# Performance work log

Hardware: AMD Instinct MI355X
Metric: run time of the kernel (lower is better)

Reference implementation:

```python
import jax, jax.numpy as jnp
import numpy as np

N, C = 65536, 512
DK = C // 2
B = 1024  # crystals; L = N // B atoms per crystal
BN_EPS = 1e-5
L1_EPS = 1e-9


def setup_inputs() -> dict:
    key = jax.random.key(0)
    ks = jax.random.split(key, 4)
    s = 1.0 / np.sqrt(C)
    return {
        "atom_fea": jax.random.normal(ks[0], (N, C), jnp.float32),
        # q_conv and k_conv share weight/bias in the original module -> single Wqk
        "Wqk": jax.random.normal(ks[1], (DK, C), jnp.float32) * s,
        "bqk": jnp.zeros((DK,), jnp.float32),
        "Wv": jax.random.normal(ks[2], (C, C), jnp.float32) * s,
        "bv": jnp.zeros((C,), jnp.float32),
        "Wt": jax.random.normal(ks[3], (C, C), jnp.float32) * s,
        "bt": jnp.zeros((C,), jnp.float32),
        "gamma": jnp.ones((C,), jnp.float32),
        "beta": jnp.zeros((C,), jnp.float32),
        "num_crystals": B,
    }


def reference(atom_fea, Wqk, bqk, Wv, bv, Wt, bt, gamma, beta, num_crystals):
    n, c = atom_fea.shape
    dk = Wqk.shape[0]
    b = num_crystals
    l = n // b  # atoms per crystal (equal-size segments)

    # 1x1 convs == linear projections; q and k are tied -> one projection
    qk = atom_fea @ Wqk.T + bqk          # [N, dk]
    v = atom_fea @ Wv.T + bv             # [N, C]

    qkb = qk.reshape(b, l, dk)
    vb = v.reshape(b, l, c)

    # per-crystal energy: [b, i(query), j(key)]
    energy = jnp.einsum("bid,bjd->bij", qkb, qkb) / jnp.sqrt(jnp.float32(dk))
    # softmax over dim=-2 (query axis), then L1-normalize over keys
    a = jax.nn.softmax(energy, axis=-2)
    att = a / (L1_EPS + a.sum(axis=-1, keepdims=True))

    x_r = jnp.einsum("bij,bjc->bic", att, vb).reshape(n, c)
    x_trans = atom_fea - x_r

    t = x_trans @ Wt.T + bt              # trans_conv (1x1)
    # BatchNorm1d in training mode: batch stats over the atom axis
    mean = t.mean(axis=0)
    var = t.var(axis=0)
    bn = (t - mean) * jax.lax.rsqrt(var + BN_EPS) * gamma + beta
    return atom_fea + jax.nn.relu(bn)
```

## Files before the change

### kernel.cpp

```cpp
#include <hip/hip_runtime.h>
#include <stdint.h>

#define NAT 65536
#define CH 512
#define NQKV 768

typedef __bf16 bf16x8 __attribute__((ext_vector_type(8)));
typedef float f32x4 __attribute__((ext_vector_type(4)));

union B8 { uint4 u; __bf16 h[8]; };

__device__ __forceinline__ void gload16(const void* g, void* l) {
  __builtin_amdgcn_global_load_lds((const __attribute__((address_space(1))) void*)g,
                                   (__attribute__((address_space(3))) void*)l, 16, 0, 0);
}

__global__ void k_prep(const float* __restrict__ atom, const float* __restrict__ wqk,
                       const float* __restrict__ bqk, const float* __restrict__ wv,
                       const float* __restrict__ bv, const float* __restrict__ wt,
                       __bf16* __restrict__ atom16, __bf16* __restrict__ wqkv16,
                       float* __restrict__ bqkv, __bf16* __restrict__ wt16,
                       float* __restrict__ stats)
{
  int tid = blockIdx.x * blockDim.x + threadIdx.x;
  int nth = gridDim.x * blockDim.x;
  const float4* a4 = (const float4*)atom;
  for (int i = tid; i < NAT * CH / 8; i += nth) {
    float4 x = a4[2 * i], y = a4[2 * i + 1];
    B8 u;
    u.h[0] = (__bf16)x.x; u.h[1] = (__bf16)x.y; u.h[2] = (__bf16)x.z; u.h[3] = (__bf16)x.w;
    u.h[4] = (__bf16)y.x; u.h[5] = (__bf16)y.y; u.h[6] = (__bf16)y.z; u.h[7] = (__bf16)y.w;
    ((uint4*)atom16)[i] = u.u;
  }
  for (int i = tid; i < NQKV * CH / 8; i += nth) {
    int row = (i * 8) >> 9;
    const float* src = (row < 256) ? (wqk + (size_t)i * 8) : (wv + (size_t)i * 8 - 256 * 512);
    float4 x = ((const float4*)src)[0], y = ((const float4*)src)[1];
    B8 u;
    u.h[0] = (__bf16)x.x; u.h[1] = (__bf16)x.y; u.h[2] = (__bf16)x.z; u.h[3] = (__bf16)x.w;
    u.h[4] = (__bf16)y.x; u.h[5] = (__bf16)y.y; u.h[6] = (__bf16)y.z; u.h[7] = (__bf16)y.w;
    ((uint4*)wqkv16)[i] = u.u;
  }
  for (int i = tid; i < CH * CH / 8; i += nth) {
    float4 x = ((const float4*)wt)[2 * i], y = ((const float4*)wt)[2 * i + 1];
    B8 u;
    u.h[0] = (__bf16)x.x; u.h[1] = (__bf16)x.y; u.h[2] = (__bf16)x.z; u.h[3] = (__bf16)x.w;
    u.h[4] = (__bf16)y.x; u.h[5] = (__bf16)y.y; u.h[6] = (__bf16)y.z; u.h[7] = (__bf16)y.w;
    ((uint4*)wt16)[i] = u.u;
  }
  if (tid < NQKV) bqkv[tid] = (tid < 256) ? bqk[tid] : bv[tid - 256];
  if (tid < 1024) stats[tid] = 0.f;
}

template<int NOUT, bool STATS>
__global__ __launch_bounds__(256, 2) void k_gemm(const __bf16* __restrict__ A,
    const __bf16* __restrict__ W, const float* __restrict__ bias,
    __bf16* __restrict__ Cout, float* __restrict__ stats)
{
  __shared__ __align__(16) char lds[32768];
  const int t = threadIdx.x, w = t >> 6, l = t & 63;
  const int wr = w >> 1, wc = w & 1;
  const int m0 = blockIdx.x * 128, n0 = blockIdx.y * 128;
  const int lsub = l >> 3;
  const int lslot = (l & 7) ^ lsub;
  f32x4 acc[4][4] = {};

  for (int kt = 0; kt < 8; ++kt) {
    const int k0 = kt * 64;
#pragma unroll
    for (int i = 0; i < 4; ++i) {
      int row = (w * 4 + i) * 8 + lsub;
      gload16(A + ((size_t)(m0 + row) * 512 + k0 + lslot * 8), lds + (w * 4 + i) * 1024);
      gload16(W + ((size_t)(n0 + row) * 512 + k0 + lslot * 8), lds + 16384 + (w * 4 + i) * 1024);
    }
    asm volatile("s_waitcnt vmcnt(0)" ::: "memory");
    __syncthreads();
#pragma unroll
    for (int ks = 0; ks < 2; ++ks) {
      bf16x8 af[4], bfr[4];
#pragma unroll
      for (int mi = 0; mi < 4; ++mi) {
        int r = wr * 64 + mi * 16 + (l & 15);
        int slot = (ks * 4 + (l >> 4)) ^ (r & 7);
        af[mi] = *(const bf16x8*)(lds + r * 128 + (slot << 4));
      }
#pragma unroll
      for (int ni = 0; ni < 4; ++ni) {
        int r = wc * 64 + ni * 16 + (l & 15);
        int slot = (ks * 4 + (l >> 4)) ^ (r & 7);
        bfr[ni] = *(const bf16x8*)(lds + 16384 + r * 128 + (slot << 4));
      }
#pragma unroll
      for (int mi = 0; mi < 4; ++mi)
#pragma unroll
        for (int ni = 0; ni < 4; ++ni)
          acc[mi][ni] = __builtin_amdgcn_mfma_f32_16x16x32_bf16(af[mi], bfr[ni], acc[mi][ni], 0, 0, 0);
    }
    __syncthreads();
  }

  float ssum[4] = {0, 0, 0, 0}, ssq[4] = {0, 0, 0, 0};
#pragma unroll
  for (int ni = 0; ni < 4; ++ni) {
    int col = n0 + wc * 64 + ni * 16 + (l & 15);
    float bb = bias[col];
#pragma unroll
    for (int mi = 0; mi < 4; ++mi) {
#pragma unroll
      for (int r = 0; r < 4; ++r) {
        int row = m0 + wr * 64 + mi * 16 + (l >> 4) * 4 + r;
        float v = acc[mi][ni][r] + bb;
        Cout[(size_t)row * NOUT + col] = (__bf16)v;
        if (STATS) { ssum[ni] += v; ssq[ni] += v * v; }
      }
    }
  }
  if (STATS) {
#pragma unroll
    for (int ni = 0; ni < 4; ++ni) {
      float s = ssum[ni], q = ssq[ni];
      s += __shfl_xor(s, 16, 64); q += __shfl_xor(q, 16, 64);
      s += __shfl_xor(s, 32, 64); q += __shfl_xor(q, 32, 64);
      if (l < 16) {
        int col = n0 + wc * 64 + ni * 16 + l;
        atomicAdd(&stats[col], s);
        atomicAdd(&stats[512 + col], q);
      }
    }
  }
}

__global__ __launch_bounds__(256, 2) void k_attn(const __bf16* __restrict__ qkv,
    const float* __restrict__ atom, __bf16* __restrict__ xt)
{
  __shared__ __align__(16) char sm[49920];
  float* E = (float*)(sm + 32768);
  float* colinv = (float*)(sm + 49408);
  float* rowinv = (float*)(sm + 49664);
  const int t = threadIdx.x, w = t >> 6, l = t & 63;
  const size_t g0 = (size_t)blockIdx.x * 64;

#pragma unroll
  for (int i = 0; i < 8; ++i) {
    int chunk = i * 256 + t;
    int row = chunk >> 5, slot = chunk & 31;
    uint4 d = *(const uint4*)(qkv + (g0 + row) * NQKV + slot * 8);
    *(uint4*)(sm + row * 512 + ((slot ^ (row & 7)) << 4)) = d;
  }
  __syncthreads();

  f32x4 eacc[4] = {};
#pragma unroll
  for (int kk = 0; kk < 8; ++kk) {
    int ra = 16 * w + (l & 15);
    bf16x8 af = *(const bf16x8*)(sm + ra * 512 + (((kk * 4 + (l >> 4)) ^ (ra & 7)) << 4));
#pragma unroll
    for (int nj = 0; nj < 4; ++nj) {
      int rb = 16 * nj + (l & 15);
      bf16x8 bf_ = *(const bf16x8*)(sm + rb * 512 + (((kk * 4 + (l >> 4)) ^ (rb & 7)) << 4));
      eacc[nj] = __builtin_amdgcn_mfma_f32_16x16x32_bf16(af, bf_, eacc[nj], 0, 0, 0);
    }
  }
#pragma unroll
  for (int nj = 0; nj < 4; ++nj)
#pragma unroll
    for (int r = 0; r < 4; ++r) {
      int i = 16 * w + (l >> 4) * 4 + r;
      int j = 16 * nj + (l & 15);
      E[i * 65 + j] = eacc[nj][r] * 0.0625f;
    }
  __syncthreads();

  auto stage_v = [&](int h) {
#pragma unroll
    for (int ch = 0; ch < 8; ++ch) {
      int cb = w * 64 + ch * 8;
      B8 d; d.u = *(const uint4*)(qkv + (g0 + l) * NQKV + 256 + h * 256 + cb);
#pragma unroll
      for (int e = 0; e < 8; ++e) {
        int c = cb + e;
        *(__bf16*)(sm + c * 128 + (((l >> 3) ^ (c & 7)) << 4) + (l & 7) * 2) = d.h[e];
      }
    }
  };

  auto pv_half = [&](int h) {
    f32x4 acc[4][4] = {};
#pragma unroll
    for (int ks = 0; ks < 2; ++ks) {
      bf16x8 af[4];
#pragma unroll
      for (int mi = 0; mi < 4; ++mi) {
        int i = mi * 16 + (l & 15);
        float ri = rowinv[i];
        bf16x8 a;
#pragma unroll
        for (int e = 0; e < 8; ++e) {
          int j = ks * 32 + (l >> 4) * 8 + e;
          a[e] = (__bf16)(E[i * 65 + j] * colinv[j] * ri);
        }
        af[mi] = a;
      }
#pragma unroll
      for (int nc = 0; nc < 4; ++nc) {
        int c = w * 64 + nc * 16 + (l & 15);
        int slot = (ks * 4 + (l >> 4)) ^ (c & 7);
        bf16x8 bfr = *(const bf16x8*)(sm + c * 128 + (slot << 4));
#pragma unroll
        for (int mi = 0; mi < 4; ++mi)
          acc[mi][nc] = __builtin_amdgcn_mfma_f32_16x16x32_bf16(af[mi], bfr, acc[mi][nc], 0, 0, 0);
      }
    }
#pragma unroll
    for (int mi = 0; mi < 4; ++mi)
#pragma unroll
      for (int nc = 0; nc < 4; ++nc)
#pragma unroll
        for (int r = 0; r < 4; ++r) {
          int i = mi * 16 + (l >> 4) * 4 + r;
          int c = h * 256 + w * 64 + nc * 16 + (l & 15);
          size_t idx = (g0 + i) * CH + c;
          xt[idx] = (__bf16)(atom[idx] - acc[mi][nc][r]);
        }
  };

  stage_v(0);
  if (t < 64) {
    float m = -1e30f;
    for (int i = 0; i < 64; ++i) m = fmaxf(m, E[i * 65 + t]);
    float s = 0.f;
    for (int i = 0; i < 64; ++i) { float e = __expf(E[i * 65 + t] - m); E[i * 65 + t] = e; s += e; }
    colinv[t] = 1.f / s;
  }
  __syncthreads();
  if (t < 64) {
    float rs = 0.f;
    for (int j = 0; j < 64; ++j) rs += E[t * 65 + j] * colinv[j];
    rowinv[t] = 1.f / (1e-9f + rs);
  }
  __syncthreads();
  pv_half(0);
  __syncthreads();
  stage_v(1);
  __syncthreads();
  pv_half(1);
}

__global__ void k_stats(const float* __restrict__ stats, const float* __restrict__ gamma,
                        const float* __restrict__ beta, float* __restrict__ ss)
{
  int c = threadIdx.x;
  float mean = stats[c] * (1.f / NAT);
  float var = stats[512 + c] * (1.f / NAT) - mean * mean;
  float sc = gamma[c] * rsqrtf(var + 1e-5f);
  ss[c] = sc;
  ss[512 + c] = beta[c] - mean * sc;
}

__global__ void k_final(const float* __restrict__ atom, const __bf16* __restrict__ tmat,
                        const float* __restrict__ ss, float* __restrict__ out)
{
  int tid = blockIdx.x * blockDim.x + threadIdx.x;
  int nth = gridDim.x * blockDim.x;
  for (int i = tid; i < NAT * CH / 8; i += nth) {
    int colb = (i & 63) * 8;
    B8 tv; tv.u = ((const uint4*)tmat)[i];
    float4 a0 = ((const float4*)atom)[2 * i], a1 = ((const float4*)atom)[2 * i + 1];
    float4 s0 = *(const float4*)(ss + colb), s1 = *(const float4*)(ss + colb + 4);
    float4 h0 = *(const float4*)(ss + 512 + colb), h1 = *(const float4*)(ss + 512 + colb + 4);
    float4 o0, o1;
    o0.x = a0.x + fmaxf(0.f, (float)tv.h[0] * s0.x + h0.x);
    o0.y = a0.y + fmaxf(0.f, (float)tv.h[1] * s0.y + h0.y);
    o0.z = a0.z + fmaxf(0.f, (float)tv.h[2] * s0.z + h0.z);
    o0.w = a0.w + fmaxf(0.f, (float)tv.h[3] * s0.w + h0.w);
    o1.x = a1.x + fmaxf(0.f, (float)tv.h[4] * s1.x + h1.x);
    o1.y = a1.y + fmaxf(0.f, (float)tv.h[5] * s1.y + h1.y);
    o1.z = a1.z + fmaxf(0.f, (float)tv.h[6] * s1.z + h1.z);
    o1.w = a1.w + fmaxf(0.f, (float)tv.h[7] * s1.w + h1.w);
    ((float4*)out)[2 * i] = o0;
    ((float4*)out)[2 * i + 1] = o1;
  }
}

extern "C" void kernel_launch(void* const* d_in, const int* in_sizes, int n_in,
                              void* d_out, int out_size, void* d_ws, size_t ws_size,
                              hipStream_t stream) {
  const float* atom  = (const float*)d_in[0];
  const float* wqk   = (const float*)d_in[1];
  const float* bqk   = (const float*)d_in[2];
  const float* wv    = (const float*)d_in[3];
  const float* bv    = (const float*)d_in[4];
  const float* wt    = (const float*)d_in[5];
  const float* bt    = (const float*)d_in[6];
  const float* gamma = (const float*)d_in[7];
  const float* beta  = (const float*)d_in[8];
  char* ws = (char*)d_ws;

  __bf16* atom16 = (__bf16*)(ws);
  __bf16* xtr    = (__bf16*)(ws);
  __bf16* qkv    = (__bf16*)(ws + 67108864);
  __bf16* tmat   = (__bf16*)(ws + 67108864);
  __bf16* wqkv16 = (__bf16*)(ws + 167772160);
  __bf16* wt16   = (__bf16*)(ws + 168558592);
  float*  bqkv   = (float*)(ws + 169082880);
  float*  stats  = (float*)(ws + 169085952);
  float*  ss     = (float*)(ws + 169090048);
  float*  out    = (float*)d_out;

  k_prep<<<dim3(2048), dim3(256), 0, stream>>>(atom, wqk, bqk, wv, bv, wt,
                                               atom16, wqkv16, bqkv, wt16, stats);
  k_gemm<NQKV, false><<<dim3(512, 6), dim3(256), 0, stream>>>(atom16, wqkv16, bqkv, qkv, nullptr);
  k_attn<<<dim3(1024), dim3(256), 0, stream>>>(qkv, atom, xtr);
  k_gemm<CH, true><<<dim3(512, 4), dim3(256), 0, stream>>>(xtr, wt16, bt, tmat, stats);
  k_stats<<<dim3(1), dim3(512), 0, stream>>>(stats, gamma, beta, ss);
  k_final<<<dim3(2048), dim3(256), 0, stream>>>(atom, tmat, ss, out);
}
```

Before: 532.3 us.

## Double-buffer GEMM LDS loads, stage epilogue via LDS, read bf16 atoms in attention

The GEMM kernel now uses two LDS buffers so the global-to-LDS loads for the next K tile are issued while MFMAs run on the current one. Partial vmcnt waits and raw barriers replace the full drain and sync each iteration. The epilogue writes results into swizzled LDS and then stores full 16-byte rows, replacing scattered 2-byte global stores. The attention kernel subtracts from the bf16 copy of atom_fea instead of the fp32 input, halving that read traffic at some cost in precision. LDS use per GEMM block doubles to 64KB.

After: 529.5 us. Within noise of the previous version (-0.5%).

```diff
diff --git a/kernel.cpp b/kernel.cpp
--- a/kernel.cpp
+++ b/kernel.cpp
@@ -57,7 +57,7 @@
     const __bf16* __restrict__ W, const float* __restrict__ bias,
     __bf16* __restrict__ Cout, float* __restrict__ stats)
 {
-  __shared__ __align__(16) char lds[32768];
+  __shared__ __align__(16) char lds[65536];
   const int t = threadIdx.x, w = t >> 6, l = t & 63;
   const int wr = w >> 1, wc = w & 1;
   const int m0 = blockIdx.x * 128, n0 = blockIdx.y * 128;
@@ -65,16 +65,30 @@
   const int lslot = (l & 7) ^ lsub;
   f32x4 acc[4][4] = {};
 
-  for (int kt = 0; kt < 8; ++kt) {
+  auto stage = [&](int kt, int p) {
     const int k0 = kt * 64;
+    char* base = lds + p * 32768;
 #pragma unroll
     for (int i = 0; i < 4; ++i) {
       int row = (w * 4 + i) * 8 + lsub;
-      gload16(A + ((size_t)(m0 + row) * 512 + k0 + lslot * 8), lds + (w * 4 + i) * 1024);
-      gload16(W + ((size_t)(n0 + row) * 512 + k0 + lslot * 8), lds + 16384 + (w * 4 + i) * 1024);
-    }
-    asm volatile("s_waitcnt vmcnt(0)" ::: "memory");
-    __syncthreads();
+      gload16(A + ((size_t)(m0 + row) * 512 + k0 + lslot * 8), base + (w * 4 + i) * 1024);
+      gload16(W + ((size_t)(n0 + row) * 512 + k0 + lslot * 8), base + 16384 + (w * 4 + i) * 1024);
+    }
+  };
+
+  stage(0, 0);
+#pragma unroll
+  for (int kt = 0; kt < 8; ++kt) {
+    const int p = kt & 1;
+    if (kt < 7) {
+      stage(kt + 1, p ^ 1);
+      asm volatile("s_waitcnt vmcnt(8)" ::: "memory");
+    } else {
+      asm volatile("s_waitcnt vmcnt(0)" ::: "memory");
+    }
+    __builtin_amdgcn_s_barrier();
+    __builtin_amdgcn_sched_barrier(0);
+    const char* base = lds + p * 32768;
 #pragma unroll
     for (int ks = 0; ks < 2; ++ks) {
       bf16x8 af[4], bfr[4];
@@ -82,13 +96,13 @@
       for (int mi = 0; mi < 4; ++mi) {
         int r = wr * 64 + mi * 16 + (l & 15);
         int slot = (ks * 4 + (l >> 4)) ^ (r & 7);
-        af[mi] = *(const bf16x8*)(lds + r * 128 + (slot << 4));
+        af[mi] = *(const bf16x8*)(base + r * 128 + (slot << 4));
       }
 #pragma unroll
       for (int ni = 0; ni < 4; ++ni) {
         int r = wc * 64 + ni * 16 + (l & 15);
         int slot = (ks * 4 + (l >> 4)) ^ (r & 7);
-        bfr[ni] = *(const bf16x8*)(lds + 16384 + r * 128 + (slot << 4));
+        bfr[ni] = *(const bf16x8*)(base + 16384 + r * 128 + (slot << 4));
       }
 #pragma unroll
       for (int mi = 0; mi < 4; ++mi)
@@ -96,24 +110,38 @@
         for (int ni = 0; ni < 4; ++ni)
           acc[mi][ni] = __builtin_amdgcn_mfma_f32_16x16x32_bf16(af[mi], bfr[ni], acc[mi][ni], 0, 0, 0);
     }
-    __syncthreads();
-  }
-
+    if (kt < 7) {
+      asm volatile("s_waitcnt lgkmcnt(0)" ::: "memory");
+      __builtin_amdgcn_s_barrier();
+    }
+  }
+
+  float bb[4];
+#pragma unroll
+  for (int ni = 0; ni < 4; ++ni) bb[ni] = bias[n0 + wc * 64 + ni * 16 + (l & 15)];
   float ssum[4] = {0, 0, 0, 0}, ssq[4] = {0, 0, 0, 0};
 #pragma unroll
   for (int ni = 0; ni < 4; ++ni) {
-    int col = n0 + wc * 64 + ni * 16 + (l & 15);
-    float bb = bias[col];
 #pragma unroll
     for (int mi = 0; mi < 4; ++mi) {
 #pragma unroll
       for (int r = 0; r < 4; ++r) {
-        int row = m0 + wr * 64 + mi * 16 + (l >> 4) * 4 + r;
-        float v = acc[mi][ni][r] + bb;
-        Cout[(size_t)row * NOUT + col] = (__bf16)v;
+        int row = wr * 64 + mi * 16 + (l >> 4) * 4 + r;
+        int col = wc * 64 + ni * 16 + (l & 15);
+        float v = acc[mi][ni][r] + bb[ni];
         if (STATS) { ssum[ni] += v; ssq[ni] += v * v; }
-      }
-    }
+        int s = col >> 3;
+        *(__bf16*)(lds + row * 256 + ((s ^ ((row >> 2) & 15)) << 4) + (col & 7) * 2) = (__bf16)v;
+      }
+    }
+  }
+  __syncthreads();
+#pragma unroll
+  for (int j = 0; j < 8; ++j) {
+    int chunk = j * 256 + t;
+    int row = chunk >> 4, sp = chunk & 15;
+    uint4 d = *(const uint4*)(lds + row * 256 + ((sp ^ ((row >> 2) & 15)) << 4));
+    *(uint4*)(Cout + (size_t)(m0 + row) * NOUT + n0 + sp * 8) = d;
   }
   if (STATS) {
 #pragma unroll
@@ -131,7 +159,7 @@
 }
 
 __global__ __launch_bounds__(256, 2) void k_attn(const __bf16* __restrict__ qkv,
-    const float* __restrict__ atom, __bf16* __restrict__ xt)
+    const __bf16* __restrict__ atom16, __bf16* __restrict__ xt)
 {
   __shared__ __align__(16) char sm[49920];
   float* E = (float*)(sm + 32768);
@@ -220,7 +248,8 @@
           int i = mi * 16 + (l >> 4) * 4 + r;
           int c = h * 256 + w * 64 + nc * 16 + (l & 15);
           size_t idx = (g0 + i) * CH + c;
-          xt[idx] = (__bf16)(atom[idx] - acc[mi][nc][r]);
+          float av = (float)atom16[idx];
+          xt[idx] = (__bf16)(av - acc[mi][nc][r]);
         }
   };
 
@@ -310,7 +339,7 @@
   k_prep<<<dim3(2048), dim3(256), 0, stream>>>(atom, wqk, bqk, wv, bv, wt,
                                                atom16, wqkv16, bqkv, wt16, stats);
   k_gemm<NQKV, false><<<dim3(512, 6), dim3(256), 0, stream>>>(atom16, wqkv16, bqkv, qkv, nullptr);
-  k_attn<<<dim3(1024), dim3(256), 0, stream>>>(qkv, atom, xtr);
+  k_attn<<<dim3(1024), dim3(256), 0, stream>>>(qkv, atom16, xtr);
   k_gemm<CH, true><<<dim3(512, 4), dim3(256), 0, stream>>>(xtr, wt16, bt, tmat, stats);
   k_stats<<<dim3(1), dim3(512), 0, stream>>>(stats, gamma, beta, ss);
   k_final<<<dim3(2048), dim3(256), 0, stream>>>(atom, tmat, ss, out);
```

## Widen GEMM tiles, parallelize attention softmax, stage attention output through LDS

Applied to the files above, without the earlier changes.

The projection GEMMs now use 512-thread blocks computing 128x256 tiles, with B fragments loaded per column step to cut register pressure and raise operand reuse. In the attention kernel, the column softmax and row L1 sums are spread over all 256 threads with shuffle reductions, where only one wave did this serially before. The P·V result is staged through LDS so the residual subtraction uses coalesced 16-byte reads and writes, and it reads the bf16 atom copy instead of fp32. This aims to cut serial softmax time and scattered 2-byte global traffic. The cost is an extra LDS round trip with added barriers, and a residual computed from the bf16 input.

Result: faster. 476.0 us (-10.6%).

```diff
diff --git a/kernel.cpp b/kernel.cpp
--- a/kernel.cpp
+++ b/kernel.cpp
@@ -53,48 +53,48 @@
 }
 
 template<int NOUT, bool STATS>
-__global__ __launch_bounds__(256, 2) void k_gemm(const __bf16* __restrict__ A,
+__global__ __launch_bounds__(512, 4) void k_gemm(const __bf16* __restrict__ A,
     const __bf16* __restrict__ W, const float* __restrict__ bias,
     __bf16* __restrict__ Cout, float* __restrict__ stats)
 {
-  __shared__ __align__(16) char lds[32768];
+  __shared__ __align__(16) char lds[49152];
   const int t = threadIdx.x, w = t >> 6, l = t & 63;
-  const int wr = w >> 1, wc = w & 1;
-  const int m0 = blockIdx.x * 128, n0 = blockIdx.y * 128;
-  const int lsub = l >> 3;
-  const int lslot = (l & 7) ^ lsub;
+  const int wr = w >> 2, wc = w & 3;
+  const int m0 = blockIdx.x * 128, n0 = blockIdx.y * 256;
+  const int lrow = l >> 3;
+  const int lslot = (l & 7) ^ lrow;
   f32x4 acc[4][4] = {};
 
   for (int kt = 0; kt < 8; ++kt) {
     const int k0 = kt * 64;
 #pragma unroll
+    for (int i = 0; i < 2; ++i) {
+      int row = (i * 8 + w) * 8 + lrow;
+      gload16(A + ((size_t)(m0 + row) * 512 + k0 + lslot * 8), lds + (i * 8 + w) * 1024);
+    }
+#pragma unroll
     for (int i = 0; i < 4; ++i) {
-      int row = (w * 4 + i) * 8 + lsub;
-      gload16(A + ((size_t)(m0 + row) * 512 + k0 + lslot * 8), lds + (w * 4 + i) * 1024);
-      gload16(W + ((size_t)(n0 + row) * 512 + k0 + lslot * 8), lds + 16384 + (w * 4 + i) * 1024);
+      int row = (i * 8 + w) * 8 + lrow;
+      gload16(W + ((size_t)(n0 + row) * 512 + k0 + lslot * 8), lds + 16384 + (i * 8 + w) * 1024);
     }
     asm volatile("s_waitcnt vmcnt(0)" ::: "memory");
     __syncthreads();
 #pragma unroll
     for (int ks = 0; ks < 2; ++ks) {
-      bf16x8 af[4], bfr[4];
+      bf16x8 af[4];
 #pragma unroll
       for (int mi = 0; mi < 4; ++mi) {
         int r = wr * 64 + mi * 16 + (l & 15);
-        int slot = (ks * 4 + (l >> 4)) ^ (r & 7);
-        af[mi] = *(const bf16x8*)(lds + r * 128 + (slot << 4));
+        af[mi] = *(const bf16x8*)(lds + r * 128 + (((ks * 4 + (l >> 4)) ^ (r & 7)) << 4));
       }
 #pragma unroll
       for (int ni = 0; ni < 4; ++ni) {
         int r = wc * 64 + ni * 16 + (l & 15);
-        int slot = (ks * 4 + (l >> 4)) ^ (r & 7);
-        bfr[ni] = *(const bf16x8*)(lds + 16384 + r * 128 + (slot << 4));
-      }
-#pragma unroll
-      for (int mi = 0; mi < 4; ++mi)
-#pragma unroll
-        for (int ni = 0; ni < 4; ++ni)
-          acc[mi][ni] = __builtin_amdgcn_mfma_f32_16x16x32_bf16(af[mi], bfr[ni], acc[mi][ni], 0, 0, 0);
+        bf16x8 bfr = *(const bf16x8*)(lds + 16384 + r * 128 + (((ks * 4 + (l >> 4)) ^ (r & 7)) << 4));
+#pragma unroll
+        for (int mi = 0; mi < 4; ++mi)
+          acc[mi][ni] = __builtin_amdgcn_mfma_f32_16x16x32_bf16(af[mi], bfr, acc[mi][ni], 0, 0, 0);
+      }
     }
     __syncthreads();
   }
@@ -131,7 +131,7 @@
 }
 
 __global__ __launch_bounds__(256, 2) void k_attn(const __bf16* __restrict__ qkv,
-    const float* __restrict__ atom, __bf16* __restrict__ xt)
+    const __bf16* __restrict__ atom16, __bf16* __restrict__ xt)
 {
   __shared__ __align__(16) char sm[49920];
   float* E = (float*)(sm + 32768);
@@ -184,7 +184,35 @@
     }
   };
 
-  auto pv_half = [&](int h) {
+  stage_v(0);
+
+  {
+    int j = t >> 2, sub = t & 3;
+    float m = -1e30f;
+#pragma unroll
+    for (int k = 0; k < 16; ++k) m = fmaxf(m, E[(sub + 4 * k) * 65 + j]);
+    m = fmaxf(m, __shfl_xor(m, 1)); m = fmaxf(m, __shfl_xor(m, 2));
+    float s = 0.f;
+#pragma unroll
+    for (int k = 0; k < 16; ++k) {
+      float e = __expf(E[(sub + 4 * k) * 65 + j] - m);
+      E[(sub + 4 * k) * 65 + j] = e; s += e;
+    }
+    s += __shfl_xor(s, 1); s += __shfl_xor(s, 2);
+    if (sub == 0) colinv[j] = 1.f / s;
+  }
+  __syncthreads();
+  {
+    int i = t >> 2, sub = t & 3;
+    float rs = 0.f;
+#pragma unroll
+    for (int k = 0; k < 16; ++k) { int j = sub + 4 * k; rs += E[i * 65 + j] * colinv[j]; }
+    rs += __shfl_xor(rs, 1); rs += __shfl_xor(rs, 2);
+    if (sub == 0) rowinv[i] = 1.f / (1e-9f + rs);
+  }
+  __syncthreads();
+
+  auto pv_out = [&](int h) {
     f32x4 acc[4][4] = {};
 #pragma unroll
     for (int ks = 0; ks < 2; ++ks) {
@@ -204,13 +232,13 @@
 #pragma unroll
       for (int nc = 0; nc < 4; ++nc) {
         int c = w * 64 + nc * 16 + (l & 15);
-        int slot = (ks * 4 + (l >> 4)) ^ (c & 7);
-        bf16x8 bfr = *(const bf16x8*)(sm + c * 128 + (slot << 4));
+        bf16x8 bfr = *(const bf16x8*)(sm + c * 128 + (((ks * 4 + (l >> 4)) ^ (c & 7)) << 4));
 #pragma unroll
         for (int mi = 0; mi < 4; ++mi)
           acc[mi][nc] = __builtin_amdgcn_mfma_f32_16x16x32_bf16(af[mi], bfr, acc[mi][nc], 0, 0, 0);
       }
     }
+    __syncthreads();
 #pragma unroll
     for (int mi = 0; mi < 4; ++mi)
 #pragma unroll
@@ -218,32 +246,30 @@
 #pragma unroll
         for (int r = 0; r < 4; ++r) {
           int i = mi * 16 + (l >> 4) * 4 + r;
-          int c = h * 256 + w * 64 + nc * 16 + (l & 15);
-          size_t idx = (g0 + i) * CH + c;
-          xt[idx] = (__bf16)(atom[idx] - acc[mi][nc][r]);
+          int c = w * 64 + nc * 16 + (l & 15);
+          int s = c >> 3;
+          *(__bf16*)(sm + i * 512 + (((s ^ (i & 7))) << 4) + (c & 7) * 2) = (__bf16)acc[mi][nc][r];
         }
+    __syncthreads();
+#pragma unroll
+    for (int j = 0; j < 8; ++j) {
+      int chunk = j * 256 + t;
+      int row = chunk >> 5, p = chunk & 31;
+      int s = p ^ (row & 7);
+      B8 xv; xv.u = *(const uint4*)(sm + row * 512 + p * 16);
+      B8 av; av.u = *(const uint4*)(atom16 + (g0 + row) * 512 + h * 256 + s * 8);
+      B8 o;
+#pragma unroll
+      for (int e = 0; e < 8; ++e) o.h[e] = (__bf16)((float)av.h[e] - (float)xv.h[e]);
+      *(uint4*)(xt + (g0 + row) * 512 + h * 256 + s * 8) = o.u;
+    }
   };
 
-  stage_v(0);
-  if (t < 64) {
-    float m = -1e30f;
-    for (int i = 0; i < 64; ++i) m = fmaxf(m, E[i * 65 + t]);
-    float s = 0.f;
-    for (int i = 0; i < 64; ++i) { float e = __expf(E[i * 65 + t] - m); E[i * 65 + t] = e; s += e; }
-    colinv[t] = 1.f / s;
-  }
-  __syncthreads();
-  if (t < 64) {
-    float rs = 0.f;
-    for (int j = 0; j < 64; ++j) rs += E[t * 65 + j] * colinv[j];
-    rowinv[t] = 1.f / (1e-9f + rs);
-  }
-  __syncthreads();
-  pv_half(0);
+  pv_out(0);
   __syncthreads();
   stage_v(1);
   __syncthreads();
-  pv_half(1);
+  pv_out(1);
 }
 
 __global__ void k_stats(const float* __restrict__ stats, const float* __restrict__ gamma,
@@ -309,9 +335,9 @@
 
   k_prep<<<dim3(2048), dim3(256), 0, stream>>>(atom, wqk, bqk, wv, bv, wt,
                                                atom16, wqkv16, bqkv, wt16, stats);
-  k_gemm<NQKV, false><<<dim3(512, 6), dim3(256), 0, stream>>>(atom16, wqkv16, bqkv, qkv, nullptr);
-  k_attn<<<dim3(1024), dim3(256), 0, stream>>>(qkv, atom, xtr);
-  k_gemm<CH, true><<<dim3(512, 4), dim3(256), 0, stream>>>(xtr, wt16, bt, tmat, stats);
+  k_gemm<NQKV, false><<<dim3(512, 3), dim3(512), 0, stream>>>(atom16, wqkv16, bqkv, qkv, nullptr);
+  k_attn<<<dim3(1024), dim3(256), 0, stream>>>(qkv, atom16, xtr);
+  k_gemm<CH, true><<<dim3(512, 2), dim3(512), 0, stream>>>(xtr, wt16, bt, tmat, stats);
   k_stats<<<dim3(1), dim3(512), 0, stream>>>(stats, gamma, beta, ss);
   k_final<<<dim3(2048), dim3(256), 0, stream>>>(atom, tmat, ss, out);
 }
```
